# Kernel optimization log

Measured on AMD Instinct MI355X. Metric: run time of the kernel, lower is better.

Reference implementation:

```python
import jax, jax.numpy as jnp
import numpy as np

MODES1 = 20
MODES2 = 20
WIDTH = 64
NUM_LAYERS = 4
B, H, W = 8, 256, 256


def _conv2d(x, w, b, pad):
    # x: (B,C,H,W), w: (O,I,kh,kw)
    y = jax.lax.conv_general_dilated(
        x, w, window_strides=(1, 1), padding=[(pad, pad), (pad, pad)],
        dimension_numbers=('NCHW', 'OIHW', 'NCHW'))
    return y + b[None, :, None, None]


def _spectral_conv(x, w1, w2, m1, m2):
    # x: (B,C,H,W); w1,w2: (I,O,m1,m2,2) real/imag pairs
    h, w = x.shape[-2], x.shape[-1]
    x_ft = jnp.fft.rfft2(x, norm='ortho')              # (B,C,H,W//2+1) complex
    w1c = w1[..., 0] + 1j * w1[..., 1]
    w2c = w2[..., 0] + 1j * w2[..., 1]
    top = jnp.einsum('bixy,ioxy->boxy', x_ft[:, :, :m1, :m2], w1c)
    bot = jnp.einsum('bixy,ioxy->boxy', x_ft[:, :, -m1:, :m2], w2c)
    out_ft = jnp.zeros((x.shape[0], w1.shape[1], h, w // 2 + 1), dtype=x_ft.dtype)
    out_ft = out_ft.at[:, :, :m1, :m2].set(top)
    out_ft = out_ft.at[:, :, -m1:, :m2].set(bot)
    return jnp.fft.irfft2(out_ft, s=(h, w), norm='ortho')


def setup_inputs() -> dict:
    key = jax.random.key(0)
    ks = jax.random.split(key, 16)
    C = WIDTH
    L = NUM_LAYERS
    scale = 1.0 / (C * C)
    inp = {
        'x': jax.random.normal(ks[0], (B, H, W, 3), dtype=jnp.float32),
        'fc0_w': jax.random.normal(ks[1], (3, C), dtype=jnp.float32) * 0.1,
        'fc0_b': jnp.zeros((C,), dtype=jnp.float32),
        'w1': scale * jax.random.uniform(ks[2], (L, C, C, MODES1, MODES2, 2), dtype=jnp.float32),
        'w2': scale * jax.random.uniform(ks[3], (L, C, C, MODES1, MODES2, 2), dtype=jnp.float32),
        'convh_w': jax.random.normal(ks[4], (L, C, C, 3, 3), dtype=jnp.float32) * 0.02,
        'convh_b': jnp.zeros((L, C), dtype=jnp.float32),
        'convw_w': jax.random.normal(ks[5], (L, C, C, 3, 3), dtype=jnp.float32) * 0.02,
        'convw_b': jnp.zeros((L, C), dtype=jnp.float32),
        'pw_w': jax.random.normal(ks[6], (L, C, C, 1, 1), dtype=jnp.float32) * 0.05,
        'pw_b': jnp.zeros((L, C), dtype=jnp.float32),
        'fc1_w': jax.random.normal(ks[7], (C, 128), dtype=jnp.float32) * 0.05,
        'fc1_b': jnp.zeros((128,), dtype=jnp.float32),
        'fc2_w': jax.random.normal(ks[8], (128, 1), dtype=jnp.float32) * 0.05,
        'fc2_b': jnp.zeros((1,), dtype=jnp.float32),
    }
    return inp


def reference(x, fc0_w, fc0_b, w1, w2, convh_w, convh_b, convw_w, convw_b,
              pw_w, pw_b, fc1_w, fc1_b, fc2_w, fc2_b):
    # fc0 lift: (B,H,W,3) -> (B,H,W,C) -> (B,C,H,W)
    h = jnp.einsum('bhwc,cd->bhwd', x, fc0_w) + fc0_b
    h = jnp.transpose(h, (0, 3, 1, 2))
    for i in range(NUM_LAYERS):
        x1 = _spectral_conv(h, w1[i], w2[i], MODES1, MODES2)
        # Mamba fallback block: two 3x3 convs summed (LayerNorm unused in forward)
        x2 = _conv2d(h, convh_w[i], convh_b[i], 1) + _conv2d(h, convw_w[i], convw_b[i], 1)
        x3 = _conv2d(h, pw_w[i], pw_b[i], 0)
        h = x1 + x2 + x3
        if i < NUM_LAYERS - 1:
            h = jax.nn.gelu(h, approximate=False)
    h = jnp.transpose(h, (0, 2, 3, 1))                  # (B,H,W,C)
    h = jnp.einsum('bhwc,cd->bhwd', h, fc1_w) + fc1_b
    h = jax.nn.gelu(h, approximate=False)
    out = jnp.einsum('bhwc,cd->bhwd', h, fc2_w) + fc2_b  # (B,H,W,1)
    return out
```

## Files before the change

kernel.cpp:

```cpp
#include <hip/hip_runtime.h>
#include <math.h>

#define NB 8
#define NC 64
#define NH 256
#define NW 256
#define NM 40
#define NKX 20
#define NL 4

typedef _Float16 f16x8 __attribute__((ext_vector_type(8)));
typedef float    f32x4 __attribute__((ext_vector_type(4)));

#define PERCB_FLOATS ((size_t)(2*4194304 + 655360 + 2*102400))
#define FIXED_FLOATS ((size_t)(6553600 + 10240 + 20480 + 147456 + 256 + 155648))

static __device__ __forceinline__ float gelu_f(float v) {
  return 0.5f * v * (1.f + erff(v * 0.70710678118654752f));
}
static __device__ __forceinline__ unsigned pack2(_Float16 a, _Float16 b) {
  union { _Float16 h[2]; unsigned u; } x; x.h[0] = a; x.h[1] = b; return x.u;
}

__global__ __launch_bounds__(256) void k_tables(float2* __restrict__ Tx,
                                                float2* __restrict__ Ty) {
  int t = blockIdx.x * 256 + threadIdx.x;
  const float w = (float)(2.0 * 3.14159265358979323846 / 256.0);
  if (t < NKX * 256) {
    int kx = t >> 8, x = t & 255;
    float th = (float)((kx * x) & 255) * w;
    Tx[t] = make_float2(cosf(th), sinf(th));
  }
  int u = t - NKX * 256;
  if (u >= 0 && u < NM * 256) {
    int m = u >> 8, y = u & 255;
    int ky = (m < 20) ? m : (m + 216);
    float th = (float)((ky * y) & 255) * w;
    Ty[u] = make_float2(cosf(th), sinf(th));
  }
}

__global__ __launch_bounds__(256) void k_wc(const float* __restrict__ ch,
                                            const float* __restrict__ cw,
                                            const float* __restrict__ pw,
                                            const float* __restrict__ chb,
                                            const float* __restrict__ cwb,
                                            const float* __restrict__ pwb,
                                            float* __restrict__ wc,
                                            float* __restrict__ bc) {
  int t = blockIdx.x * 256 + threadIdx.x;
  if (t < NL * NC * NC * 9) {
    int tap = t % 9;
    int io  = t / 9;
    int o   = io % 64;
    int i   = (io / 64) % 64;
    int l   = io / 4096;
    int src = ((l * 64 + o) * 64 + i) * 9 + tap;
    float v = ch[src] + cw[src];
    if (tap == 4) v += pw[(l * 64 + o) * 64 + i];
    wc[t] = v;
  }
  if (t < NL * NC) bc[t] = chb[t] + cwb[t] + pwb[t];
}

__global__ __launch_bounds__(256) void k_wpack(const float* __restrict__ wc,
                                               _Float16* __restrict__ whi,
                                               _Float16* __restrict__ wlo) {
  int t = blockIdx.x * 256 + threadIdx.x;
  int lane = t & 63;
  int nt   = (t >> 6) & 3;
  int chunk = (t >> 8) % 18;
  int l4   = t / 4608;
  int tap = chunk >> 1, half = chunk & 1;
  int o = nt * 16 + (lane & 15);
  _Float16 hi[8], lo[8];
  #pragma unroll
  for (int j = 0; j < 8; ++j) {
    int i = half * 32 + ((lane >> 4) << 3) + j;
    float v = wc[((l4 * 64 + i) * 64 + o) * 9 + tap];
    _Float16 h = (_Float16)v;
    hi[j] = h;
    lo[j] = (_Float16)(v - (float)h);
  }
  *(f16x8*)(whi + (size_t)t * 8) = *(f16x8*)hi;
  *(f16x8*)(wlo + (size_t)t * 8) = *(f16x8*)lo;
}

__global__ __launch_bounds__(256) void k_hpack(const float* __restrict__ w1,
                                               _Float16* __restrict__ whi,
                                               _Float16* __restrict__ wlo) {
  int t = blockIdx.x * 256 + threadIdx.x;
  int lane = t & 63;
  int nt   = (t >> 6) & 7;
  int chunk = t >> 9;
  int jo = nt * 16 + (lane & 15);
  _Float16 hi[8], lo[8];
  #pragma unroll
  for (int j = 0; j < 8; ++j) {
    int c = chunk * 32 + ((lane >> 4) << 3) + j;
    float v = w1[c * 128 + jo];
    _Float16 h = (_Float16)v;
    hi[j] = h;
    lo[j] = (_Float16)(v - (float)h);
  }
  *(f16x8*)(whi + (size_t)t * 8) = *(f16x8*)hi;
  *(f16x8*)(wlo + (size_t)t * 8) = *(f16x8*)lo;
}

__global__ __launch_bounds__(256) void k_fc0(const float* __restrict__ x,
                                             const float* __restrict__ w,
                                             const float* __restrict__ b,
                                             float* __restrict__ h, int b0) {
  int t = blockIdx.x * 256 + threadIdx.x;
  int ch = t & 63;
  int px = t >> 6;
  const float* xp = x + ((size_t)b0 * 65536 + px) * 3;
  h[t] = xp[0] * w[ch] + xp[1] * w[64 + ch] + xp[2] * w[128 + ch] + b[ch];
}

__global__ __launch_bounds__(256) void k_fwdx(const float* __restrict__ h,
                                              const float2* __restrict__ Tx,
                                              float2* __restrict__ Fx) {
  int bidx = blockIdx.x;
  int y  = bidx & 255;
  int bb = bidx >> 8;
  int w  = threadIdx.x >> 6;
  int ch = threadIdx.x & 63;
  const float* hp = h + ((size_t)bb * 65536 + y * 256) * 64 + ch;
  float ar[5] = {0,0,0,0,0}, ai[5] = {0,0,0,0,0};
  #pragma unroll 4
  for (int x = 0; x < 256; x += 2) {
    float v0 = hp[(size_t)x * 64];
    float v1 = hp[(size_t)(x + 1) * 64];
    #pragma unroll
    for (int q = 0; q < 5; ++q) {
      int kx = w * 5 + q;
      float4 t4 = *(const float4*)(Tx + kx * 256 + x);
      ar[q] += v0 * t4.x + v1 * t4.z;
      ai[q] -= v0 * t4.y + v1 * t4.w;
    }
  }
  float2* fp = Fx + ((size_t)(bb * 64 + ch) * 256 + y) * 20;
  #pragma unroll
  for (int q = 0; q < 5; ++q) fp[w * 5 + q] = make_float2(ar[q], ai[q]);
}

__global__ __launch_bounds__(256) void k_fwdy(const float2* __restrict__ Fx,
                                              const float2* __restrict__ Ty,
                                              float2* __restrict__ Fxy) {
  int t  = blockIdx.x * 256 + threadIdx.x;
  int kx = t % 20;
  int m  = (t / 20) % 40;
  int bc = t / 800;
  const float2* fp = Fx + (size_t)bc * NH * 20 + kx;
  const float2* tp = Ty + m * 256;
  float re = 0.f, im = 0.f;
  #pragma unroll 4
  for (int y = 0; y < 256; ++y) {
    float2 f = fp[y * 20];
    float2 w = tp[y];
    re += f.x * w.x + f.y * w.y;
    im += f.y * w.x - f.x * w.y;
  }
  Fxy[t] = make_float2(re * (1.f / 256.f), im * (1.f / 256.f));
}

__global__ __launch_bounds__(256) void k_wT(const float* __restrict__ w1,
                                            const float* __restrict__ w2,
                                            float2* __restrict__ wT, int l) {
  __shared__ float2 tile[32][33];
  int mk0 = blockIdx.x * 32;
  int io0 = blockIdx.y * 32;
  int tx = threadIdx.x & 31, ty0 = threadIdx.x >> 5;
  #pragma unroll
  for (int s = 0; s < 4; ++s) {
    int ty = ty0 * 4 + s;
    int mk = mk0 + tx, io = io0 + ty;
    int m = mk / 20, kx = mk % 20;
    const float* src = (m < 20) ? w1 : w2;
    int mm = (m < 20) ? m : (m - 20);
    size_t idx = ((((size_t)l * 4096 + io) * 20 + mm) * 20 + kx) * 2;
    tile[ty][tx] = make_float2(src[idx], src[idx + 1]);
  }
  __syncthreads();
  #pragma unroll
  for (int s = 0; s < 4; ++s) {
    int ty = ty0 * 4 + s;
    wT[(size_t)(mk0 + ty) * 4096 + (io0 + tx)] = tile[tx][ty];
  }
}

__global__ __launch_bounds__(256) void k_mix(const float2* __restrict__ Fxy,
                                             const float2* __restrict__ wT,
                                             float2* __restrict__ G, int nrows) {
  __shared__ float2 sf[512];
  int mk = blockIdx.x;
  for (int t = threadIdx.x; t < nrows; t += 256) sf[t] = Fxy[(size_t)t * 800 + mk];
  __syncthreads();
  const float2* wp = wT + (size_t)mk * 4096;
  for (int t = threadIdx.x; t < nrows; t += 256) {
    int b = t >> 6, o = t & 63;
    const float2* fb = sf + b * 64;
    float re = 0.f, im = 0.f;
    #pragma unroll 8
    for (int i = 0; i < 64; ++i) {
      float2 f = fb[i];
      float2 w = wp[i * 64 + o];
      re += f.x * w.x - f.y * w.y;
      im += f.x * w.y + f.y * w.x;
    }
    G[(size_t)(b * 64 + o) * 800 + mk] = make_float2(re, im);
  }
}

__global__ __launch_bounds__(256) void k_invy(const float2* __restrict__ G,
                                              const float2* __restrict__ Ty,
                                              float2* __restrict__ Gy) {
  int t  = blockIdx.x * 256 + threadIdx.x;
  int kx = t % 20;
  int y  = (t / 20) & 255;
  int bc = t / 5120;
  const float2* gp = G + (size_t)bc * 800 + kx;
  float re = 0.f, im = 0.f;
  #pragma unroll 4
  for (int m = 0; m < 40; ++m) {
    float2 g = gp[m * 20];
    float2 w = Ty[m * 256 + y];
    re += g.x * w.x - g.y * w.y;
    im += g.x * w.y + g.y * w.x;
  }
  Gy[t] = make_float2(re, im);
}

__global__ __launch_bounds__(256, 3) void k_conv(const float* __restrict__ hin,
                                                 const f16x8* __restrict__ wph,
                                                 const f16x8* __restrict__ wpl,
                                                 const float* __restrict__ bcb,
                                                 const float2* __restrict__ Gy,
                                                 const float2* __restrict__ Tx,
                                                 float* __restrict__ hout,
                                                 int dogelu) {
  __shared__ unsigned sAu[13056];
  int bidx = blockIdx.x;
  int xt = bidx & 7;
  int yt = (bidx >> 3) & 63;
  int bb = bidx >> 9;
  int x0 = xt << 5, y0 = yt << 2;
  int tid = threadIdx.x;
  int w = tid >> 6, lane = tid & 63, quad = lane >> 4, l15 = lane & 15;

  for (int e = tid; e < 204 * 32; e += 256) {
    int px = e >> 5, chp = e & 31;
    int rg = px / 34, cg = px % 34;
    int gy = y0 - 1 + rg, gx = x0 - 1 + cg;
    float2 v = make_float2(0.f, 0.f);
    if (gy >= 0 && gy < 256 && gx >= 0 && gx < 256)
      v = *(const float2*)(hin + (((size_t)bb * 256 + gy) * 256 + gx) * 64 + chp * 2);
    _Float16 h0 = (_Float16)v.x, h1 = (_Float16)v.y;
    _Float16 l0 = (_Float16)(v.x - (float)h0), l1 = (_Float16)(v.y - (float)h1);
    int dw = (px << 5) + (chp ^ ((px & 7) << 2));
    sAu[dw] = pack2(h0, h1);
    sAu[6528 + dw] = pack2(l0, l1);
  }
  __syncthreads();

  f32x4 acc[2][4];
  #pragma unroll
  for (int s = 0; s < 2; ++s)
    #pragma unroll
    for (int nt = 0; nt < 4; ++nt) acc[s][nt] = (f32x4){0.f, 0.f, 0.f, 0.f};

  #pragma unroll 1
  for (int tap = 0; tap < 9; ++tap) {
    int dy = tap / 3, dx = tap % 3;
    #pragma unroll
    for (int half = 0; half < 2; ++half) {
      int chunk = tap * 2 + half;
      const f16x8* bh = wph + (size_t)(chunk * 4) * 64 + lane;
      const f16x8* bl = wpl + (size_t)(chunk * 4) * 64 + lane;
      f16x8 bfh[4], bfl[4];
      #pragma unroll
      for (int nt = 0; nt < 4; ++nt) { bfh[nt] = bh[nt * 64]; bfl[nt] = bl[nt * 64]; }
      f16x8 afh[2], afl[2];
      #pragma unroll
      for (int s = 0; s < 2; ++s) {
        int px = (w + dy) * 34 + (s * 16 + dx) + l15;
        int dw = (px << 5) + (((half << 4) + (quad << 2)) ^ ((px & 7) << 2));
        afh[s] = *(const f16x8*)(sAu + dw);
        afl[s] = *(const f16x8*)(sAu + 6528 + dw);
      }
      #pragma unroll
      for (int s = 0; s < 2; ++s)
        #pragma unroll
        for (int nt = 0; nt < 4; ++nt) {
          acc[s][nt] = __builtin_amdgcn_mfma_f32_16x16x32_f16(afh[s], bfh[nt], acc[s][nt], 0, 0, 0);
          acc[s][nt] = __builtin_amdgcn_mfma_f32_16x16x32_f16(afh[s], bfl[nt], acc[s][nt], 0, 0, 0);
          acc[s][nt] = __builtin_amdgcn_mfma_f32_16x16x32_f16(afl[s], bfh[nt], acc[s][nt], 0, 0, 0);
        }
    }
  }

  __syncthreads();
  float2* sGy = (float2*)sAu;
  float2* sT  = (float2*)(sAu + 10496);
  for (int e = tid; e < 5120; e += 256) {
    int o = e / 80, rem = e % 80;
    int row = rem / 20, kx = rem % 20;
    sGy[o * 82 + row * 20 + kx] =
        Gy[((size_t)(bb * 64 + o) * 256 + (y0 + row)) * 20 + kx];
  }
  for (int e = tid; e < 640; e += 256) {
    int kx = e >> 5, col = e & 31;
    sT[e] = Tx[kx * 256 + x0 + col];
  }
  __syncthreads();

  const float scale = 1.f / 256.f;
  #pragma unroll
  for (int s = 0; s < 2; ++s) {
    int colb = s * 16 + (quad << 2);
    #pragma unroll
    for (int nt = 0; nt < 4; ++nt) {
      int o = nt * 16 + l15;
      float bias = bcb[o];
      const float2* gp = sGy + o * 82 + w * 20;
      f32x4 sr = {0.f, 0.f, 0.f, 0.f};
      #pragma unroll
      for (int p = 0; p < 10; ++p) {
        float4 g = *(const float4*)(gp + 2 * p);
        float f0 = (p == 0) ? 1.f : 2.f;
        float4 tA = *(const float4*)(sT + (2 * p) * 32 + colb);
        float4 tB = *(const float4*)(sT + (2 * p) * 32 + colb + 2);
        sr.x += f0 * (g.x * tA.x - g.y * tA.y);
        sr.y += f0 * (g.x * tA.z - g.y * tA.w);
        sr.z += f0 * (g.x * tB.x - g.y * tB.y);
        sr.w += f0 * (g.x * tB.z - g.y * tB.w);
        float4 tC = *(const float4*)(sT + (2 * p + 1) * 32 + colb);
        float4 tD = *(const float4*)(sT + (2 * p + 1) * 32 + colb + 2);
        sr.x += 2.f * (g.z * tC.x - g.w * tC.y);
        sr.y += 2.f * (g.z * tC.z - g.w * tC.w);
        sr.z += 2.f * (g.z * tD.x - g.w * tD.y);
        sr.w += 2.f * (g.z * tD.z - g.w * tD.w);
      }
      #pragma unroll
      for (int r = 0; r < 4; ++r) {
        float v = acc[s][nt][r] + bias + sr[r] * scale;
        if (dogelu) v = gelu_f(v);
        int xcol = x0 + colb + r;
        hout[(((size_t)bb * 256 + (y0 + w)) * 256 + xcol) * 64 + o] = v;
      }
    }
  }
}

__global__ __launch_bounds__(256, 2) void k_head(const float* __restrict__ h,
                                                 const f16x8* __restrict__ whi,
                                                 const f16x8* __restrict__ wlo,
                                                 const float* __restrict__ b1,
                                                 const float* __restrict__ w2,
                                                 const float* __restrict__ b2,
                                                 float* __restrict__ out, int b0) {
  int tid = threadIdx.x;
  int w = tid >> 6, lane = tid & 63, quad = lane >> 4, l15 = lane & 15;
  int px0 = blockIdx.x * 64 + w * 16;

  f32x4 acc[8];
  #pragma unroll
  for (int nt = 0; nt < 8; ++nt) acc[nt] = (f32x4){0.f, 0.f, 0.f, 0.f};

  #pragma unroll
  for (int half = 0; half < 2; ++half) {
    const float* ap = h + (size_t)(px0 + l15) * 64 + half * 32 + quad * 8;
    float4 a0 = *(const float4*)ap;
    float4 a1 = *(const float4*)(ap + 4);
    _Float16 ah[8], al[8];
    float av[8] = {a0.x, a0.y, a0.z, a0.w, a1.x, a1.y, a1.z, a1.w};
    #pragma unroll
    for (int j = 0; j < 8; ++j) {
      ah[j] = (_Float16)av[j];
      al[j] = (_Float16)(av[j] - (float)ah[j]);
    }
    f16x8 afh = *(f16x8*)ah, afl = *(f16x8*)al;
    #pragma unroll
    for (int nt = 0; nt < 8; ++nt) {
      f16x8 bh = whi[(size_t)(half * 8 + nt) * 64 + lane];
      f16x8 bl = wlo[(size_t)(half * 8 + nt) * 64 + lane];
      acc[nt] = __builtin_amdgcn_mfma_f32_16x16x32_f16(afh, bh, acc[nt], 0, 0, 0);
      acc[nt] = __builtin_amdgcn_mfma_f32_16x16x32_f16(afh, bl, acc[nt], 0, 0, 0);
      acc[nt] = __builtin_amdgcn_mfma_f32_16x16x32_f16(afl, bh, acc[nt], 0, 0, 0);
    }
  }

  float part[4] = {0.f, 0.f, 0.f, 0.f};
  #pragma unroll
  for (int nt = 0; nt < 8; ++nt) {
    int jo = nt * 16 + l15;
    float bb1 = b1[jo], ww2 = w2[jo];
    #pragma unroll
    for (int r = 0; r < 4; ++r)
      part[r] += gelu_f(acc[nt][r] + bb1) * ww2;
  }
  #pragma unroll
  for (int r = 0; r < 4; ++r) {
    float v = part[r];
    v += __shfl_xor(v, 1);
    v += __shfl_xor(v, 2);
    v += __shfl_xor(v, 4);
    v += __shfl_xor(v, 8);
    if (l15 == 0)
      out[(size_t)b0 * 65536 + px0 + quad * 4 + r] = v + b2[0];
  }
}

extern "C" void kernel_launch(void* const* d_in, const int* in_sizes, int n_in,
                              void* d_out, int out_size, void* d_ws, size_t ws_size,
                              hipStream_t stream) {
  const float* x    = (const float*)d_in[0];
  const float* fc0w = (const float*)d_in[1];
  const float* fc0b = (const float*)d_in[2];
  const float* w1   = (const float*)d_in[3];
  const float* w2   = (const float*)d_in[4];
  const float* chw  = (const float*)d_in[5];
  const float* chb  = (const float*)d_in[6];
  const float* cww  = (const float*)d_in[7];
  const float* cwb  = (const float*)d_in[8];
  const float* pww  = (const float*)d_in[9];
  const float* pwb  = (const float*)d_in[10];
  const float* fc1w = (const float*)d_in[11];
  const float* fc1b = (const float*)d_in[12];
  const float* fc2w = (const float*)d_in[13];
  const float* fc2b = (const float*)d_in[14];

  int cb = 1;
  for (int cand = 8; cand >= 1; cand >>= 1) {
    size_t need = (PERCB_FLOATS * (size_t)cand + FIXED_FLOATS) * sizeof(float);
    if (ws_size >= need) { cb = cand; break; }
  }

  const size_t szH = (size_t)cb * 4194304;

  float*  ws  = (float*)d_ws;
  float*  h   = ws;
  float*  h2  = h + szH;
  float2* Fx  = (float2*)(h2 + szH);
  float2* Fxy = (float2*)((float*)Fx + (size_t)cb * 655360);
  float2* G   = (float2*)((float*)Fxy + (size_t)cb * 102400);
  float2* wT  = (float2*)((float*)G + (size_t)cb * 102400);
  float2* Tx  = (float2*)((float*)wT + 6553600);
  float2* Ty  = (float2*)((float*)Tx + 10240);
  float*  wcb = (float*)Ty + 20480;
  float*  bcb = wcb + 147456;
  _Float16* wpkhi = (_Float16*)(bcb + 256);
  _Float16* wpklo = wpkhi + 147456;
  _Float16* w1hi  = wpklo + 147456;
  _Float16* w1lo  = w1hi + 8192;
  float2* Gy = Fx;

  k_tables<<<60, 256, 0, stream>>>(Tx, Ty);
  k_wc<<<576, 256, 0, stream>>>(chw, cww, pww, chb, cwb, pwb, wcb, bcb);
  k_wpack<<<72, 256, 0, stream>>>(wcb, wpkhi, wpklo);
  k_hpack<<<4, 256, 0, stream>>>(fc1w, w1hi, w1lo);

  for (int b0 = 0; b0 < NB; b0 += cb) {
    k_fc0<<<cb * 16384, 256, 0, stream>>>(x, fc0w, fc0b, h, b0);
    float* cur = h;
    float* nxt = h2;
    for (int l = 0; l < NL; ++l) {
      k_fwdx<<<cb * 256, 256, 0, stream>>>(cur, Tx, Fx);
      k_fwdy<<<cb * 200, 256, 0, stream>>>(Fx, Ty, Fxy);
      k_wT<<<dim3(25, 128), 256, 0, stream>>>(w1, w2, wT, l);
      k_mix<<<NM * NKX, 256, 0, stream>>>(Fxy, wT, G, cb * 64);
      k_invy<<<cb * 1280, 256, 0, stream>>>(G, Ty, Gy);
      k_conv<<<cb * 512, 256, 0, stream>>>(cur,
                                           (const f16x8*)(wpkhi + (size_t)l * 36864),
                                           (const f16x8*)(wpklo + (size_t)l * 36864),
                                           bcb + (size_t)l * 64, Gy, Tx, nxt,
                                           (l < NL - 1) ? 1 : 0);
      float* tmp = cur; cur = nxt; nxt = tmp;
    }
    k_head<<<cb * 1024, 256, 0, stream>>>(cur, (const f16x8*)w1hi, (const f16x8*)w1lo,
                                          fc1b, fc2w, fc2b, (float*)d_out, b0);
  }
}
```

Before: 4.930 ms.

## Stage FFT inputs in LDS, transpose Fxy layout, and coalesce conv output stores

k_fwdx now loads the whole 64KB row of h into shared memory with float4 loads before the DFT loop. k_fwdy switches to one block per (batch, channel), stages that channel's Fx slice in LDS, and writes its output transposed so k_mix can read it contiguously. The k_conv epilogue handles 32 output channels at a time and routes results through an LDS transpose buffer so the writes to hout become coalesced float4 stores. The aim is fewer strided global accesses, paid for with more shared memory (which may lower occupancy) and extra barriers.

```diff
diff --git a/kernel.cpp b/kernel.cpp
--- a/kernel.cpp
+++ b/kernel.cpp
@@ -121,17 +121,21 @@
 __global__ __launch_bounds__(256) void k_fwdx(const float* __restrict__ h,
                                               const float2* __restrict__ Tx,
                                               float2* __restrict__ Fx) {
+  __shared__ float sm[16384];
   int bidx = blockIdx.x;
   int y  = bidx & 255;
   int bb = bidx >> 8;
+  const float* hp = h + ((size_t)bb * 65536 + y * 256) * 64;
+  for (int e = threadIdx.x; e < 4096; e += 256)
+    *(float4*)(sm + e * 4) = *(const float4*)(hp + e * 4);
+  __syncthreads();
   int w  = threadIdx.x >> 6;
   int ch = threadIdx.x & 63;
-  const float* hp = h + ((size_t)bb * 65536 + y * 256) * 64 + ch;
   float ar[5] = {0,0,0,0,0}, ai[5] = {0,0,0,0,0};
   #pragma unroll 4
   for (int x = 0; x < 256; x += 2) {
-    float v0 = hp[(size_t)x * 64];
-    float v1 = hp[(size_t)(x + 1) * 64];
+    float v0 = sm[x * 64 + ch];
+    float v1 = sm[x * 64 + 64 + ch];
     #pragma unroll
     for (int q = 0; q < 5; ++q) {
       int kx = w * 5 + q;
@@ -147,22 +151,26 @@
 
 __global__ __launch_bounds__(256) void k_fwdy(const float2* __restrict__ Fx,
                                               const float2* __restrict__ Ty,
-                                              float2* __restrict__ Fxy) {
-  int t  = blockIdx.x * 256 + threadIdx.x;
-  int kx = t % 20;
-  int m  = (t / 20) % 40;
-  int bc = t / 800;
-  const float2* fp = Fx + (size_t)bc * NH * 20 + kx;
-  const float2* tp = Ty + m * 256;
-  float re = 0.f, im = 0.f;
-  #pragma unroll 4
-  for (int y = 0; y < 256; ++y) {
-    float2 f = fp[y * 20];
-    float2 w = tp[y];
-    re += f.x * w.x + f.y * w.y;
-    im += f.y * w.x - f.x * w.y;
-  }
-  Fxy[t] = make_float2(re * (1.f / 256.f), im * (1.f / 256.f));
+                                              float2* __restrict__ FxyT, int nbc) {
+  __shared__ float2 sFx[5120];
+  int bc = blockIdx.x;
+  const float4* src = (const float4*)(Fx + (size_t)bc * 5120);
+  float4* dst = (float4*)sFx;
+  for (int e = threadIdx.x; e < 2560; e += 256) dst[e] = src[e];
+  __syncthreads();
+  for (int mk = threadIdx.x; mk < 800; mk += 256) {
+    int kx = mk % 20, m = mk / 20;
+    const float2* tp = Ty + m * 256;
+    float re = 0.f, im = 0.f;
+    #pragma unroll 4
+    for (int yy = 0; yy < 256; ++yy) {
+      float2 f = sFx[yy * 20 + kx];
+      float2 wv = tp[yy];
+      re += f.x * wv.x + f.y * wv.y;
+      im += f.y * wv.x - f.x * wv.y;
+    }
+    FxyT[(size_t)mk * nbc + bc] = make_float2(re * (1.f / 256.f), im * (1.f / 256.f));
+  }
 }
 
 __global__ __launch_bounds__(256) void k_wT(const float* __restrict__ w1,
@@ -190,12 +198,13 @@
   }
 }
 
-__global__ __launch_bounds__(256) void k_mix(const float2* __restrict__ Fxy,
+__global__ __launch_bounds__(256) void k_mix(const float2* __restrict__ FxyT,
                                              const float2* __restrict__ wT,
                                              float2* __restrict__ G, int nrows) {
   __shared__ float2 sf[512];
   int mk = blockIdx.x;
-  for (int t = threadIdx.x; t < nrows; t += 256) sf[t] = Fxy[(size_t)t * 800 + mk];
+  for (int t = threadIdx.x; t < nrows; t += 256)
+    sf[t] = FxyT[(size_t)mk * nrows + t];
   __syncthreads();
   const float2* wp = wT + (size_t)mk * 4096;
   for (int t = threadIdx.x; t < nrows; t += 256) {
@@ -301,54 +310,69 @@
   }
 
   __syncthreads();
-  float2* sGy = (float2*)sAu;
-  float2* sT  = (float2*)(sAu + 10496);
-  for (int e = tid; e < 5120; e += 256) {
-    int o = e / 80, rem = e % 80;
-    int row = rem / 20, kx = rem % 20;
-    sGy[o * 82 + row * 20 + kx] =
-        Gy[((size_t)(bb * 64 + o) * 256 + (y0 + row)) * 20 + kx];
-  }
+  float2* sT  = (float2*)sAu;
+  float2* sGy = (float2*)(sAu + 1280);
+  float*  sTr = (float*)(sAu + 6528);
   for (int e = tid; e < 640; e += 256) {
     int kx = e >> 5, col = e & 31;
     sT[e] = Tx[kx * 256 + x0 + col];
   }
-  __syncthreads();
-
   const float scale = 1.f / 256.f;
-  #pragma unroll
-  for (int s = 0; s < 2; ++s) {
-    int colb = s * 16 + (quad << 2);
-    #pragma unroll
-    for (int nt = 0; nt < 4; ++nt) {
-      int o = nt * 16 + l15;
+  #pragma unroll 1
+  for (int oh = 0; oh < 2; ++oh) {
+    __syncthreads();
+    for (int e = tid; e < 2560; e += 256) {
+      int ol = e / 80, rem = e % 80;
+      int row = rem / 20, kx = rem % 20;
+      sGy[ol * 82 + row * 20 + kx] =
+          Gy[((size_t)(bb * 64 + oh * 32 + ol) * 256 + (y0 + row)) * 20 + kx];
+    }
+    __syncthreads();
+    #pragma unroll
+    for (int nt2 = 0; nt2 < 2; ++nt2) {
+      int nt = oh * 2 + nt2;
+      int ol = nt2 * 16 + l15;
+      int o  = oh * 32 + ol;
       float bias = bcb[o];
-      const float2* gp = sGy + o * 82 + w * 20;
-      f32x4 sr = {0.f, 0.f, 0.f, 0.f};
+      const float2* gp = sGy + ol * 82 + w * 20;
       #pragma unroll
-      for (int p = 0; p < 10; ++p) {
-        float4 g = *(const float4*)(gp + 2 * p);
-        float f0 = (p == 0) ? 1.f : 2.f;
-        float4 tA = *(const float4*)(sT + (2 * p) * 32 + colb);
-        float4 tB = *(const float4*)(sT + (2 * p) * 32 + colb + 2);
-        sr.x += f0 * (g.x * tA.x - g.y * tA.y);
-        sr.y += f0 * (g.x * tA.z - g.y * tA.w);
-        sr.z += f0 * (g.x * tB.x - g.y * tB.y);
-        sr.w += f0 * (g.x * tB.z - g.y * tB.w);
-        float4 tC = *(const float4*)(sT + (2 * p + 1) * 32 + colb);
-        float4 tD = *(const float4*)(sT + (2 * p + 1) * 32 + colb + 2);
-        sr.x += 2.f * (g.z * tC.x - g.w * tC.y);
-        sr.y += 2.f * (g.z * tC.z - g.w * tC.w);
-        sr.z += 2.f * (g.z * tD.x - g.w * tD.y);
-        sr.w += 2.f * (g.z * tD.z - g.w * tD.w);
+      for (int s = 0; s < 2; ++s) {
+        int colb = s * 16 + (quad << 2);
+        f32x4 sr = {0.f, 0.f, 0.f, 0.f};
+        #pragma unroll
+        for (int p = 0; p < 10; ++p) {
+          float4 g = *(const float4*)(gp + 2 * p);
+          float f0 = (p == 0) ? 1.f : 2.f;
+          float4 tA = *(const float4*)(sT + (2 * p) * 32 + colb);
+          float4 tB = *(const float4*)(sT + (2 * p) * 32 + colb + 2);
+          sr.x += f0 * (g.x * tA.x - g.y * tA.y);
+          sr.y += f0 * (g.x * tA.z - g.y * tA.w);
+          sr.z += f0 * (g.x * tB.x - g.y * tB.y);
+          sr.w += f0 * (g.x * tB.z - g.y * tB.w);
+          float4 tC = *(const float4*)(sT + (2 * p + 1) * 32 + colb);
+          float4 tD = *(const float4*)(sT + (2 * p + 1) * 32 + colb + 2);
+          sr.x += 2.f * (g.z * tC.x - g.w * tC.y);
+          sr.y += 2.f * (g.z * tC.z - g.w * tC.w);
+          sr.z += 2.f * (g.z * tD.x - g.w * tD.y);
+          sr.w += 2.f * (g.z * tD.z - g.w * tD.w);
+        }
+        #pragma unroll
+        for (int r = 0; r < 4; ++r) {
+          float v = acc[s][nt][r] + bias + sr[r] * scale;
+          if (dogelu) v = gelu_f(v);
+          sTr[(w * 32 + s * 16 + (quad << 2) + r) * 36 + ol] = v;
+        }
       }
-      #pragma unroll
-      for (int r = 0; r < 4; ++r) {
-        float v = acc[s][nt][r] + bias + sr[r] * scale;
-        if (dogelu) v = gelu_f(v);
-        int xcol = x0 + colb + r;
-        hout[(((size_t)bb * 256 + (y0 + w)) * 256 + xcol) * 64 + o] = v;
-      }
+    }
+    __syncthreads();
+    #pragma unroll
+    for (int k = 0; k < 4; ++k) {
+      int e = tid + k * 256;
+      int P = e >> 3, sub = e & 7;
+      float4 v4 = *(const float4*)(sTr + P * 36 + sub * 4);
+      int row = P >> 5, px32 = P & 31;
+      *(float4*)(hout + (((size_t)bb * 256 + (y0 + row)) * 256 + x0 + px32) * 64
+                 + oh * 32 + sub * 4) = v4;
     }
   }
 }
@@ -465,11 +489,12 @@
     k_fc0<<<cb * 16384, 256, 0, stream>>>(x, fc0w, fc0b, h, b0);
     float* cur = h;
     float* nxt = h2;
+    int nbc = cb * 64;
     for (int l = 0; l < NL; ++l) {
       k_fwdx<<<cb * 256, 256, 0, stream>>>(cur, Tx, Fx);
-      k_fwdy<<<cb * 200, 256, 0, stream>>>(Fx, Ty, Fxy);
+      k_fwdy<<<nbc, 256, 0, stream>>>(Fx, Ty, Fxy, nbc);
       k_wT<<<dim3(25, 128), 256, 0, stream>>>(w1, w2, wT, l);
-      k_mix<<<NM * NKX, 256, 0, stream>>>(Fxy, wT, G, cb * 64);
+      k_mix<<<NM * NKX, 256, 0, stream>>>(Fxy, wT, G, nbc);
       k_invy<<<cb * 1280, 256, 0, stream>>>(G, Ty, Gy);
       k_conv<<<cb * 512, 256, 0, stream>>>(cur,
                                            (const f16x8*)(wpkhi + (size_t)l * 36864),
```

Result: faster. 4.770 ms (-3.2%).
